# Optimization experiments

Hardware: AMD Instinct MI355X
Metric: run time of the kernel (lower is better)

## Reference

```python
import jax, jax.numpy as jnp
import numpy as np

N_HEAD = 16


def setup_inputs() -> dict:
    key = jax.random.key(0)
    ks = jax.random.split(key, 6)
    B, T, C = 2, 2048, 1024
    x = jax.random.normal(ks[0], (B, T, C), dtype=jnp.float32)
    # causal mask, broadcastable over [B, H, T, T]
    attn_mask = jnp.tril(jnp.ones((T, T), dtype=jnp.int32))[None, None]
    s = 1.0 / np.sqrt(C)
    W_attn = jax.random.normal(ks[1], (C, 3 * C), dtype=jnp.float32) * s
    b_attn = jnp.zeros((3 * C,), dtype=jnp.float32)
    W_proj = jax.random.normal(ks[2], (C, C), dtype=jnp.float32) * s
    b_proj = jnp.zeros((C,), dtype=jnp.float32)
    return {"x": x, "attn_mask": attn_mask, "W_attn": W_attn,
            "b_attn": b_attn, "W_proj": W_proj, "b_proj": b_proj}


def reference(x, attn_mask, W_attn, b_attn, W_proj, b_proj):
    B, T, C = x.shape
    H = N_HEAD
    D = C // H
    qkv = x @ W_attn + b_attn                      # [B, T, 3C]
    q, k, v = jnp.split(qkv, 3, axis=-1)
    q = q.reshape(B, T, H, D).transpose(0, 2, 1, 3)  # [B, H, T, D]
    k = k.reshape(B, T, H, D).transpose(0, 2, 1, 3)
    v = v.reshape(B, T, H, D).transpose(0, 2, 1, 3)
    att = jnp.einsum('bhtd,bhsd->bhts', q, k) * (1.0 / np.sqrt(D))
    att = jnp.where(attn_mask == 0, jnp.float32(-jnp.inf), att)
    att = jax.nn.softmax(att, axis=-1)             # [B, H, T, T]
    y = jnp.einsum('bhts,bhsd->bhtd', att, v)      # [B, H, T, D]
    y = y.transpose(0, 2, 1, 3).reshape(B, T, C)
    y = y @ W_proj + b_proj
    return y
```

## Files before the change

kernel.cpp:

```cpp
#include <hip/hip_runtime.h>
#include <hip/hip_bf16.h>
#include <stdint.h>

#define H_NUM 16
#define DH 64
#define TSEQ 2048
#define CDIM 1024

typedef short shortx8 __attribute__((ext_vector_type(8)));
typedef float f32x4 __attribute__((ext_vector_type(4)));
typedef unsigned short u16;
typedef unsigned int u32;
typedef unsigned long long u64;

#define MFMA16(a,b,c) __builtin_amdgcn_mfma_f32_16x16x32_bf16(a,b,c,0,0,0)

static __device__ __forceinline__ u16 f2bf(float f) {
  union { float f; u32 u; } v; v.f = f;
  u32 r = v.u + 0x7fffu + ((v.u >> 16) & 1u);
  return (u16)(r >> 16);
}
static __device__ __forceinline__ float bf2f(u16 b) {
  union { u32 u; float f; } v; v.u = ((u32)b) << 16;
  return v.f;
}

static __device__ __forceinline__ void gload_lds16(const void* g, void* l) {
  __builtin_amdgcn_global_load_lds(
    (const __attribute__((address_space(1))) void*)g,
    (__attribute__((address_space(3))) void*)l, 16, 0, 0);
}

extern "C" __global__ __launch_bounds__(1024) void k_prep(
    const float* __restrict__ x, u16* __restrict__ xb,
    const float* __restrict__ Wa, u16* __restrict__ wat,
    const float* __restrict__ Wp, u16* __restrict__ wpt)
{
  __shared__ float t[32][33];
  int bid = blockIdx.x, tid = threadIdx.x;
  if (bid < 1024) {
    int i = bid * 1024 + tid;
    float4 v = ((const float4*)x)[i];
    union { u16 h[4]; uint2 u; } o;
    o.h[0] = f2bf(v.x); o.h[1] = f2bf(v.y); o.h[2] = f2bf(v.z); o.h[3] = f2bf(v.w);
    ((uint2*)xb)[i] = o.u;
    return;
  }
  const float* in; u16* out; int Ccols, bx, by;
  if (bid < 4096) { int tt = bid - 1024; in = Wa; out = wat; Ccols = 3072; bx = tt % 96; by = tt / 96; }
  else            { int tt = bid - 4096; in = Wp; out = wpt; Ccols = 1024; bx = tt & 31; by = tt >> 5; }
  int tx = tid & 31, ty = tid >> 5;
  int c0 = bx * 32, r0 = by * 32;
  t[ty][tx] = in[(size_t)(r0 + ty) * Ccols + c0 + tx];
  __syncthreads();
  out[(size_t)(c0 + ty) * 1024 + r0 + tx] = f2bf(t[tx][ty]);
}

template<int OUT_BF16>
__global__ __launch_bounds__(256) void k_gemm_bt(
    const u16* __restrict__ A, const u16* __restrict__ Bt,
    const float* __restrict__ bias, void* __restrict__ Cout,
    int M, int N, int K)
{
  __shared__ u16 lds_a[2][128 * 32];
  __shared__ u16 lds_b[2][128 * 32];
  int tid = threadIdx.x;
  int w = tid >> 6, l = tid & 63;
  int lg = l >> 4, lr = l & 15;
  int nwg = gridDim.x * gridDim.y;
  int lin = blockIdx.y * gridDim.x + blockIdx.x;
  int cpx = nwg >> 3;
  int swz = (lin & 7) * cpx + (lin >> 3);
  int m0 = (swz / gridDim.x) * 128, n0 = (swz % gridDim.x) * 128;
  int wm = w >> 1, wn = w & 1;
  f32x4 acc[4][4];
#pragma unroll
  for (int i = 0; i < 4; ++i)
#pragma unroll
    for (int j = 0; j < 4; ++j) acc[i][j] = (f32x4){0.f, 0.f, 0.f, 0.f};

  auto STAGE = [&](int k0, int buf) {
#pragma unroll
    for (int j = 0; j < 2; ++j) {
      int ci = w * 2 + j;
      gload_lds16(A  + (size_t)(m0 + ci * 16 + (l >> 2)) * K + k0 + (l & 3) * 8,
                  (char*)lds_a[buf] + ci * 1024);
      gload_lds16(Bt + (size_t)(n0 + ci * 16 + (l >> 2)) * K + k0 + (l & 3) * 8,
                  (char*)lds_b[buf] + ci * 1024);
    }
  };

  int nt = K >> 5;
  STAGE(0, 0);
  int cur = 0;
  for (int t = 0; t < nt; ++t) {
    asm volatile("s_waitcnt vmcnt(0)" ::: "memory");
    __syncthreads();
    if (t + 1 < nt) STAGE((t + 1) << 5, cur ^ 1);
    shortx8 af[4], bf[4];
#pragma unroll
    for (int i = 0; i < 4; ++i) {
      af[i] = *(const shortx8*)((const char*)lds_a[cur] + (64 * wm + 16 * i + lr) * 64 + lg * 16);
      bf[i] = *(const shortx8*)((const char*)lds_b[cur] + (64 * wn + 16 * i + lr) * 64 + lg * 16);
    }
    __builtin_amdgcn_s_setprio(1);
#pragma unroll
    for (int mi = 0; mi < 4; ++mi)
#pragma unroll
      for (int ni = 0; ni < 4; ++ni)
        acc[mi][ni] = MFMA16(af[mi], bf[ni], acc[mi][ni]);
    __builtin_amdgcn_s_setprio(0);
    cur ^= 1;
  }
#pragma unroll
  for (int mi = 0; mi < 4; ++mi)
#pragma unroll
    for (int ni = 0; ni < 4; ++ni) {
      int col = n0 + 64 * wn + 16 * ni + lr;
      float bz = bias[col];
#pragma unroll
      for (int r = 0; r < 4; ++r) {
        int row = m0 + 64 * wm + 16 * mi + 4 * lg + r;
        float v = acc[mi][ni][r] + bz;
        if (OUT_BF16) ((u16*)Cout)[(size_t)row * N + col] = f2bf(v);
        else          ((float*)Cout)[(size_t)row * N + col] = v;
      }
    }
}

extern "C" __global__ __launch_bounds__(256) void k_transpose_v(
    const u16* __restrict__ qkv, u16* __restrict__ vt)
{
  __shared__ u16 tile[64][72];
  int bh = blockIdx.y; int b = bh >> 4, h = bh & 15;
  int t0 = blockIdx.x * 64;
  int tid = threadIdx.x;
#pragma unroll
  for (int p = 0; p < 2; ++p) {
    int tr = p * 32 + (tid >> 3), dc = (tid & 7) * 8;
    shortx8 v = *(const shortx8*)(qkv + (size_t)(b * TSEQ + t0 + tr) * 3072 + 2 * CDIM + h * DH + dc);
    *(shortx8*)&tile[tr][dc] = v;
  }
  __syncthreads();
#pragma unroll
  for (int p = 0; p < 2; ++p) {
    int dr = p * 32 + (tid >> 3), tc = (tid & 7) * 8;
    shortx8 o;
#pragma unroll
    for (int j = 0; j < 8; ++j) o[j] = (short)tile[tc + j][dr];
    *(shortx8*)(vt + (size_t)(bh * DH + dr) * TSEQ + t0 + tc) = o;
  }
}

extern "C" __global__ __launch_bounds__(256) void k_attn(
    const u16* __restrict__ qkv, const u16* __restrict__ vt, u16* __restrict__ yb)
{
  __shared__ u16 lds_k[3][64 * 64];
  __shared__ u16 lds_v[3][64 * 64];
  __shared__ u16 lds_p[4 * 1024];
  int d = blockIdx.x;
  int xcd = d & 7, j = d >> 3;
  int hb = xcd + 8 * (j >> 4);
  int bx = j & 15;
  int h = hb & 15, b = hb >> 4;
  int tid = threadIdx.x, w = tid >> 6, l = tid & 63;
  int lg = l >> 4, lr = l & 15;
  const float QSCALE = 0.18033688011112042f;
  const u16* vbase = vt + (size_t)(b * H_NUM + h) * DH * TSEQ;
  u16* pw = lds_p + w * 1024;

  auto STAGE = [&](int kv0, int buf) {
#pragma unroll
    for (int jj = 0; jj < 2; ++jj) {
      int ci = w * 2 + jj;
      int row = ci * 8 + (l >> 3);
      int a = ((l & 7) ^ (row & 7)) * 8;
      gload_lds16(qkv + (size_t)(b * TSEQ + kv0 + row) * 3072 + CDIM + h * DH + a,
                  (char*)lds_k[buf] + ci * 1024);
      gload_lds16(vbase + (size_t)row * TSEQ + kv0 + a,
                  (char*)lds_v[buf] + ci * 1024);
    }
  };

  for (int qi = 0; qi < 2; ++qi) {
    int qb = qi ? (31 - bx) : bx;
    int q0 = qb * 64;

    int qrow = q0 + 16 * w + lr;
    const u16* qp = qkv + (size_t)(b * TSEQ + qrow) * 3072 + h * DH;
    shortx8 qf[2];
#pragma unroll
    for (int s_ = 0; s_ < 2; ++s_) {
      shortx8 v = *(const shortx8*)(qp + s_ * 32 + lg * 8);
#pragma unroll
      for (int i = 0; i < 8; ++i) v[i] = (short)f2bf(bf2f((u16)v[i]) * QSCALE);
      qf[s_] = v;
    }

    f32x4 yacc[4];
#pragma unroll
    for (int i = 0; i < 4; ++i) yacc[i] = (f32x4){0.f, 0.f, 0.f, 0.f};
    float m_run[4] = {-3.0e38f, -3.0e38f, -3.0e38f, -3.0e38f};
    float l_part[4] = {0.f, 0.f, 0.f, 0.f};
    f32x4 s[4];

    auto QKT = [&](int buf) {
#pragma unroll
      for (int idx = 0; idx < 4; ++idx) s[idx] = (f32x4){0.f, 0.f, 0.f, 0.f};
      int kswz = (lr & 7) << 4;
#pragma unroll
      for (int idx = 0; idx < 4; ++idx) {
        const char* kb_ = (const char*)lds_k[buf] + (idx * 16 + lr) * 128;
#pragma unroll
        for (int d0 = 0; d0 < 2; ++d0) {
          shortx8 kf = *(const shortx8*)(kb_ + ((d0 * 64 + lg * 16) ^ kswz));
          s[idx] = MFMA16(qf[d0], kf, s[idx]);
        }
      }
    };

    auto SOFTMAX = [&](int kv0) {
      if (kv0 == q0) {
#pragma unroll
        for (int idx = 0; idx < 4; ++idx)
#pragma unroll
          for (int r = 0; r < 4; ++r) {
            int row_l = 16 * w + 4 * lg + r;
            if (idx * 16 + lr > row_l) s[idx][r] = -3.0e38f;
          }
      }
#pragma unroll
      for (int r = 0; r < 4; ++r) {
        float a0 = s[0][r], a1 = s[1][r], a2 = s[2][r], a3 = s[3][r];
        float pmax = fmaxf(fmaxf(a0, a1), fmaxf(a2, a3));
        float mr = m_run[r];
        u64 bal = __ballot(pmax > mr + 8.0f);
        if ((bal >> (lg * 16)) & 0xFFFFull) {
          float gm = pmax;
          gm = fmaxf(gm, __shfl_xor(gm, 1));
          gm = fmaxf(gm, __shfl_xor(gm, 2));
          gm = fmaxf(gm, __shfl_xor(gm, 4));
          gm = fmaxf(gm, __shfl_xor(gm, 8));
          float mn = fmaxf(mr, gm);
          float al = __builtin_amdgcn_exp2f(mr - mn);
          l_part[r] *= al;
#pragma unroll
          for (int dt = 0; dt < 4; ++dt) yacc[dt][r] *= al;
          m_run[r] = mn; mr = mn;
        }
        float p0 = __builtin_amdgcn_exp2f(a0 - mr);
        float p1 = __builtin_amdgcn_exp2f(a1 - mr);
        float p2 = __builtin_amdgcn_exp2f(a2 - mr);
        float p3 = __builtin_amdgcn_exp2f(a3 - mr);
        l_part[r] += (p0 + p1) + (p2 + p3);
        u32 pk01, pk23;
        asm("v_cvt_pk_bf16_f32 %0, %1, %2" : "=v"(pk01) : "v"(p0), "v"(p1));
        asm("v_cvt_pk_bf16_f32 %0, %1, %2" : "=v"(pk23) : "v"(p2), "v"(p3));
        int q = 4 * lg + r;
        int rb = q * 64, swq = (q & 7) << 3;
        pw[rb + ((lr)      ^ swq)] = (u16)pk01;
        pw[rb + ((16 + lr) ^ swq)] = (u16)(pk01 >> 16);
        pw[rb + ((32 + lr) ^ swq)] = (u16)pk23;
        pw[rb + ((48 + lr) ^ swq)] = (u16)(pk23 >> 16);
      }
    };

    auto PV = [&](int buf) {
      int pswz = (lr & 7) << 4;
#pragma unroll
      for (int c = 0; c < 2; ++c) {
        shortx8 pa = *(const shortx8*)((const char*)pw + lr * 128 + ((c * 64 + lg * 16) ^ pswz));
#pragma unroll
        for (int dt = 0; dt < 4; ++dt) {
          int vr = dt * 16 + lr;
          shortx8 vf = *(const shortx8*)((const char*)lds_v[buf] + vr * 128 +
                         ((c * 64 + lg * 16) ^ ((vr & 7) << 4)));
          yacc[dt] = MFMA16(pa, vf, yacc[dt]);
        }
      }
    };

    int nt = qb + 1;
    __syncthreads();
    STAGE(0, 0);
    asm volatile("s_waitcnt vmcnt(0)" ::: "memory");
    __syncthreads();
    __builtin_amdgcn_s_setprio(1);
    QKT(0);
    __builtin_amdgcn_s_setprio(0);
    if (nt > 1) STAGE(64, 1);
    SOFTMAX(0);

    int vb = 0;
    for (int t = 0; t < nt; ++t) {
      int kb = vb + 1; if (kb == 3) kb = 0;
      int st = kb + 1; if (st == 3) st = 0;
      asm volatile("s_waitcnt vmcnt(0)" ::: "memory");
      __syncthreads();
      __builtin_amdgcn_s_setprio(1);
      if (t + 1 < nt) QKT(kb);
      PV(vb);
      __builtin_amdgcn_s_setprio(0);
      if (t + 2 < nt) STAGE((t + 2) * 64, st);
      if (t + 1 < nt) SOFTMAX((t + 1) * 64);
      vb = kb;
    }

#pragma unroll
    for (int r = 0; r < 4; ++r) {
      float lsum = l_part[r];
      lsum += __shfl_xor(lsum, 1);
      lsum += __shfl_xor(lsum, 2);
      lsum += __shfl_xor(lsum, 4);
      lsum += __shfl_xor(lsum, 8);
      float inv = 1.0f / lsum;
      int row = q0 + 16 * w + 4 * lg + r;
      u16* yp = yb + (size_t)(b * TSEQ + row) * CDIM + h * DH;
#pragma unroll
      for (int dt = 0; dt < 4; ++dt)
        yp[dt * 16 + lr] = f2bf(yacc[dt][r] * inv);
    }
  }
}

extern "C" void kernel_launch(void* const* d_in, const int* in_sizes, int n_in,
                              void* d_out, int out_size, void* d_ws, size_t ws_size,
                              hipStream_t stream) {
  const float* x      = (const float*)d_in[0];
  const float* W_attn = (const float*)d_in[2];
  const float* b_attn = (const float*)d_in[3];
  const float* W_proj = (const float*)d_in[4];
  const float* b_proj = (const float*)d_in[5];

  char* ws = (char*)d_ws;
  u16* xb  = (u16*)ws;
  u16* wat = (u16*)(ws + (8ull  << 20));
  u16* wpt = (u16*)(ws + (14ull << 20));
  u16* qkv = (u16*)(ws + (16ull << 20));
  u16* vt  = (u16*)(ws + (40ull << 20));
  u16* yb  = (u16*)(ws + (48ull << 20));

  k_prep<<<dim3(5120), dim3(1024), 0, stream>>>(x, xb, W_attn, wat, W_proj, wpt);
  k_gemm_bt<1><<<dim3(24, 32), dim3(256), 0, stream>>>(xb, wat, b_attn, qkv, 4096, 3072, 1024);
  k_transpose_v<<<dim3(32, 32), dim3(256), 0, stream>>>(qkv, vt);
  k_attn<<<dim3(512), dim3(256), 0, stream>>>(qkv, vt, yb);
  k_gemm_bt<0><<<dim3(8, 32), dim3(256), 0, stream>>>(yb, wpt, b_proj, d_out, 4096, 1024, 1024);
}
```

Measured before the change: 127.0 us.

## Add 256x256-tile 8-wave pipelined GEMM for QKV projection

Replaces the 128x128 QKV GEMM with a new kernel that uses 256x256 output tiles, 512 threads (8 waves), and a multi-stage split-K LDS pipeline. Global-to-LDS loads are interleaved with MFMA phases, and s_setprio raises wave priority around the MFMA blocks. The larger tiles improve operand reuse and cut global traffic. The grid becomes 192 workgroups, which may underfill the CUs. Each thread holds 128 accumulator floats, so register pressure is high and occupancy drops.

```diff
diff --git a/kernel.cpp b/kernel.cpp
--- a/kernel.cpp
+++ b/kernel.cpp
@@ -54,6 +54,104 @@
   t[ty][tx] = in[(size_t)(r0 + ty) * Ccols + c0 + tx];
   __syncthreads();
   out[(size_t)(c0 + ty) * 1024 + r0 + tx] = f2bf(t[tx][ty]);
+}
+
+extern "C" __global__ __launch_bounds__(512) void k_gemm_8p(
+    const u16* __restrict__ A, const u16* __restrict__ Bt,
+    const float* __restrict__ bias, u16* __restrict__ Cout,
+    int M, int N, int K)
+{
+  __shared__ u16 ldsA[2][2][256 * 32];
+  __shared__ u16 ldsB[2][2][256 * 32];
+  int tid = threadIdx.x;
+  int w = tid >> 6, l = tid & 63;
+  int lg = l >> 4, lr = l & 15;
+  int wm = w >> 2, wn = w & 3;
+  int nwg = gridDim.x * gridDim.y;
+  int lin = blockIdx.y * gridDim.x + blockIdx.x;
+  int cpx = nwg >> 3;
+  int swz = (lin & 7) * cpx + (lin >> 3);
+  int m0 = (swz / gridDim.x) * 256, n0 = (swz % gridDim.x) * 256;
+
+  f32x4 acc[8][4];
+#pragma unroll
+  for (int i = 0; i < 8; ++i)
+#pragma unroll
+    for (int j = 0; j < 4; ++j) acc[i][j] = (f32x4){0.f, 0.f, 0.f, 0.f};
+
+  auto STAGE_U = [&](const u16* base, int x0, int t, int kh, u16* region) {
+#pragma unroll
+    for (int j = 0; j < 2; ++j) {
+      int row = j * 128 + (tid >> 2);
+      int c = (tid & 3) ^ ((row >> 1) & 3);
+      gload_lds16(base + (size_t)(x0 + row) * K + t * 64 + kh * 32 + c * 8,
+                  (char*)region + j * 8192 + w * 1024);
+    }
+  };
+
+  int NT = K >> 6;
+  STAGE_U(A,  m0, 0, 0, ldsA[0][0]);
+  STAGE_U(Bt, n0, 0, 0, ldsB[0][0]);
+  STAGE_U(A,  m0, 0, 1, ldsA[0][1]);
+  STAGE_U(Bt, n0, 0, 1, ldsB[0][1]);
+  STAGE_U(A,  m0, 1, 0, ldsA[1][0]);
+  STAGE_U(Bt, n0, 1, 0, ldsB[1][0]);
+  asm volatile("s_waitcnt vmcnt(8)" ::: "memory");
+  __syncthreads();
+
+  for (int T = 0; T < NT; T += 2) {
+    int t2 = (T + 2 < NT) ? T + 2 : NT - 1;
+    int t3 = (T + 3 < NT) ? T + 3 : NT - 1;
+#pragma unroll
+    for (int a = 0; a < 8; ++a) {
+      int cbuf = a >> 2;
+      int kh = (a >> 1) & 1;
+      int mh = a & 1;
+      shortx8 af[4], bfr[4];
+#pragma unroll
+      for (int mi = 0; mi < 4; ++mi) {
+        int r = wm * 128 + (mh * 4 + mi) * 16 + lr;
+        int c = lg ^ ((r >> 1) & 3);
+        af[mi] = *(const shortx8*)((const char*)ldsA[cbuf][kh] + r * 64 + c * 16);
+      }
+#pragma unroll
+      for (int ni = 0; ni < 4; ++ni) {
+        int r = wn * 64 + ni * 16 + lr;
+        int c = lg ^ ((r >> 1) & 3);
+        bfr[ni] = *(const shortx8*)((const char*)ldsB[cbuf][kh] + r * 64 + c * 16);
+      }
+      if      (a == 0) STAGE_U(A,  m0, T + 1, 1, ldsA[1][1]);
+      else if (a == 1) STAGE_U(Bt, n0, T + 1, 1, ldsB[1][1]);
+      else if (a == 2) STAGE_U(A,  m0, t2, 0, ldsA[0][0]);
+      else if (a == 3) STAGE_U(Bt, n0, t2, 0, ldsB[0][0]);
+      else if (a == 4) STAGE_U(A,  m0, t2, 1, ldsA[0][1]);
+      else if (a == 5) STAGE_U(Bt, n0, t2, 1, ldsB[0][1]);
+      else if (a == 6) STAGE_U(A,  m0, t3, 0, ldsA[1][0]);
+      else             STAGE_U(Bt, n0, t3, 0, ldsB[1][0]);
+      if (a & 1) asm volatile("s_waitcnt vmcnt(8)" ::: "memory");
+      __syncthreads();
+      __builtin_amdgcn_s_setprio(1);
+#pragma unroll
+      for (int mi = 0; mi < 4; ++mi)
+#pragma unroll
+        for (int ni = 0; ni < 4; ++ni)
+          acc[mh * 4 + mi][ni] = MFMA16(af[mi], bfr[ni], acc[mh * 4 + mi][ni]);
+      __builtin_amdgcn_s_setprio(0);
+      __syncthreads();
+    }
+  }
+#pragma unroll
+  for (int mi = 0; mi < 8; ++mi)
+#pragma unroll
+    for (int ni = 0; ni < 4; ++ni) {
+      int col = n0 + wn * 64 + ni * 16 + lr;
+      float bz = bias[col];
+#pragma unroll
+      for (int rr = 0; rr < 4; ++rr) {
+        int row = m0 + wm * 128 + mi * 16 + 4 * lg + rr;
+        Cout[(size_t)row * N + col] = f2bf(acc[mi][ni][rr] + bz);
+      }
+    }
 }
 
 template<int OUT_BF16>
@@ -341,7 +439,7 @@
   u16* yb  = (u16*)(ws + (48ull << 20));
 
   k_prep<<<dim3(5120), dim3(1024), 0, stream>>>(x, xb, W_attn, wat, W_proj, wpt);
-  k_gemm_bt<1><<<dim3(24, 32), dim3(256), 0, stream>>>(xb, wat, b_attn, qkv, 4096, 3072, 1024);
+  k_gemm_8p<<<dim3(12, 16), dim3(512), 0, stream>>>(xb, wat, b_attn, qkv, 4096, 3072, 1024);
   k_transpose_v<<<dim3(32, 32), dim3(256), 0, stream>>>(qkv, vt);
   k_attn<<<dim3(512), dim3(256), 0, stream>>>(qkv, vt, yb);
   k_gemm_bt<0><<<dim3(8, 32), dim3(256), 0, stream>>>(yb, wpt, b_proj, d_out, 4096, 1024, 1024);
```

Result: slower. 143.8 us (+13.3%).
